# Kernel tuning notes

Measured on AMD Instinct MI355X. Metric: run time of the kernel, lower is better.

Reference implementation:

```python
import jax, jax.numpy as jnp
import numpy as np

N_NODES = 100000
N_EDGES = 600000
N_GRAPHS = 512
X_DIM = 2
E_DIM = 2
U_DIM = 2


def setup_inputs() -> dict:
    key = jax.random.key(0)
    ks = jax.random.split(key, 16)
    inp = {
        "x": jax.random.normal(ks[0], (N_NODES, X_DIM), jnp.float32),
        "edge_index": jax.random.randint(ks[1], (2, N_EDGES), 0, N_NODES, jnp.int64),
        "edge_attr": jax.random.normal(ks[2], (N_EDGES, E_DIM), jnp.float32),
        "u": jax.random.normal(ks[3], (N_GRAPHS, U_DIM), jnp.float32),
        "batch": jnp.sort(jax.random.randint(ks[4], (N_NODES,), 0, N_GRAPHS, jnp.int64)),
    }
    def lin(k, fin, fout):
        bound = 1.0 / np.sqrt(fin)
        kw, kb = jax.random.split(k)
        W = jax.random.uniform(kw, (fin, fout), jnp.float32, -bound, bound)
        b = jax.random.uniform(kb, (fout,), jnp.float32, -bound, bound)
        return W, b
    inp["W1a"], inp["b1a"] = lin(ks[5], X_DIM + E_DIM, 64)
    inp["W1b"], inp["b1b"] = lin(ks[6], 64, 128)
    inp["W2a"], inp["b2a"] = lin(ks[7], X_DIM + 128 + U_DIM, 256)
    inp["W2b"], inp["b2b"] = lin(ks[8], 256, 512)
    return inp


def reference(x, edge_index, edge_attr, u, batch, W1a, b1a, W1b, b1b, W2a, b2a, W2b, b2b):
    row, col = edge_index[0], edge_index[1]
    n = x.shape[0]
    # gather + concat -> MLP1 over edges: [E, 4] -> [E, 128]
    e_in = jnp.concatenate([x[col], edge_attr], axis=1)
    h = jnp.maximum(e_in @ W1a + b1a, 0.0) @ W1b + b1b
    # scatter_mean over destination nodes (row)
    s = jax.ops.segment_sum(h, row, num_segments=n)
    cnt = jax.ops.segment_sum(jnp.ones((row.shape[0], 1), h.dtype), row, num_segments=n)
    agg = s / jnp.maximum(cnt, 1.0)
    # node-level concat -> MLP2: [N, 132] -> [N, 512]
    z = jnp.concatenate([x, agg, u[batch]], axis=1)
    return jnp.maximum(z @ W2a + b2a, 0.0) @ W2b + b2b
```

## Files before the change

kernel.cpp:

```cpp
#include <hip/hip_runtime.h>

#define NN 100000
#define NE 600000
#define NP 100096
#define NB 391
#define NBE 9375

typedef float v4    __attribute__((ext_vector_type(4)));
typedef float f32x4 __attribute__((ext_vector_type(4)));
typedef short s16x4 __attribute__((ext_vector_type(4)));
typedef short s16x8 __attribute__((ext_vector_type(8)));

__device__ __forceinline__ short f2bf(float f) {
    unsigned u = __float_as_uint(f);
    u = (u + 0x7fffu + ((u >> 16) & 1u)) >> 16;
    return (short)u;
}
__device__ __forceinline__ float bf2f(unsigned short v) {
    return __uint_as_float(((unsigned)v) << 16);
}

__global__ __launch_bounds__(256) void hist_kernel(const int* __restrict__ ei,
                                                   int* __restrict__ deg) {
    int e = blockIdx.x * 256 + threadIdx.x;
    if (e < NE) atomicAdd(&deg[ei[e]], 1);
}

__global__ __launch_bounds__(256) void scan1_kernel(const int* __restrict__ deg,
                                                    int* __restrict__ partial,
                                                    int* __restrict__ bsum) {
    __shared__ int tmp[256];
    int t = threadIdx.x;
    int i = blockIdx.x * 256 + t;
    int v = deg[i];
    tmp[t] = v;
    __syncthreads();
    for (int off = 1; off < 256; off <<= 1) {
        int add = (t >= off) ? tmp[t - off] : 0;
        __syncthreads();
        tmp[t] += add;
        __syncthreads();
    }
    partial[i] = tmp[t] - v;
    if (t == 255) bsum[blockIdx.x] = tmp[255];
}

__global__ __launch_bounds__(512) void scan2_kernel(const int* __restrict__ bsum,
                                                    int* __restrict__ boff) {
    __shared__ int tmp[512];
    int t = threadIdx.x;
    int v = (t < NB) ? bsum[t] : 0;
    tmp[t] = v;
    __syncthreads();
    for (int off = 1; off < 512; off <<= 1) {
        int add = (t >= off) ? tmp[t - off] : 0;
        __syncthreads();
        tmp[t] += add;
        __syncthreads();
    }
    boff[t] = tmp[t] - v;
}

__global__ __launch_bounds__(256) void fill_kernel(const int* __restrict__ ei,
                                                   const float* __restrict__ x,
                                                   const float* __restrict__ ea,
                                                   const int* __restrict__ partial,
                                                   const int* __restrict__ boff,
                                                   int* __restrict__ cnt2,
                                                   int* __restrict__ rowp,
                                                   short* __restrict__ in_csr) {
    int e = blockIdx.x * 256 + threadIdx.x;
    if (e < NE) {
        int r = ei[e];
        int c = ei[NE + e];
        int p = partial[r] + boff[r >> 8] + atomicAdd(&cnt2[r], 1);
        rowp[p] = r;
        s16x8 v = {0, 0, 0, 0, 0, 0, 0, 0};
        v[0] = f2bf(x[2 * c]);  v[1] = f2bf(x[2 * c + 1]);
        v[2] = f2bf(ea[2 * e]); v[3] = f2bf(ea[2 * e + 1]);
        *(s16x8*)&in_csr[(size_t)p * 8] = v;
    }
}

__global__ __launch_bounds__(256) void zero_empty_kernel(const int* __restrict__ deg,
                                                         short* __restrict__ aggb) {
    int n = blockIdx.x * 256 + threadIdx.x;
    if (n < NN && deg[n] == 0) {
        s16x8 z = {0, 0, 0, 0, 0, 0, 0, 0};
        short* dst = aggb + (size_t)n * 128;
#pragma unroll
        for (int j = 0; j < 16; ++j) *(s16x8*)&dst[j * 8] = z;
    }
}

__global__ __launch_bounds__(256) void prep_kernel(const float* __restrict__ W2a,
                                                   const float* __restrict__ W2b,
                                                   const float* __restrict__ W1a,
                                                   const float* __restrict__ W1b,
                                                   short* __restrict__ W2aF,
                                                   short* __restrict__ W2bF,
                                                   short* __restrict__ W1aT,
                                                   short* __restrict__ W1bT) {
    int idx = blockIdx.x * 256 + threadIdx.x;
    if (idx < 16 * 5 * 512) {
        int j = idx & 7;
        int lane = (idx >> 3) & 63;
        int t2 = idx >> 9;
        int ks = t2 % 5, nb = t2 / 5;
        int n = nb * 16 + (lane & 15);
        int k = ks * 32 + (lane >> 4) * 8 + j;
        float v = 0.f;
        if (k < 128)       v = W2a[(2 + k) * 256 + n];
        else if (k == 128) v = W2a[0 * 256 + n];
        else if (k == 129) v = W2a[1 * 256 + n];
        else if (k == 130) v = W2a[130 * 256 + n];
        else if (k == 131) v = W2a[131 * 256 + n];
        W2aF[idx] = f2bf(v);
    }
    if (idx < 32 * 8 * 512) {
        int j = idx & 7;
        int lane = (idx >> 3) & 63;
        int t2 = idx >> 9;
        int ks = t2 & 7, nb = t2 >> 3;
        int n = nb * 16 + (lane & 15);
        int k = ks * 32 + (lane >> 4) * 8 + j;
        W2bF[idx] = f2bf(W2b[k * 512 + n]);
    }
    if (idx < 64 * 32) {
        int n = idx >> 5, k = idx & 31;
        W1aT[idx] = (k < 4) ? f2bf(W1a[k * 64 + n]) : (short)0;
    }
    if (idx < 128 * 64) {
        int n = idx >> 6, k = idx & 63;
        W1bT[idx] = f2bf(W1b[k * 128 + n]);
    }
}

__global__ __launch_bounds__(256) void edge_fused_kernel(
    const short* __restrict__ in_csr, const int* __restrict__ rowp,
    const short* __restrict__ W1aT, const short* __restrict__ W1bT,
    const float* __restrict__ b1a, const float* __restrict__ b1b,
    const int* __restrict__ partial, const int* __restrict__ boff,
    const int* __restrict__ deg,
    short* __restrict__ aggb, float* __restrict__ pstart,
    float* __restrict__ pend, int* __restrict__ eid)
{
    __shared__ short in[64 * 48];
    __shared__ short t1[64 * 72];
    __shared__ short hbf[64 * 136];
    __shared__ int   rows[64];
    __shared__ float midlo[128], midhi[128];
    const int tid = threadIdx.x;
    const int p0 = blockIdx.x * 64;

    if (tid < 64) {
        *(s16x8*)&in[tid * 48] = *(const s16x8*)&in_csr[(size_t)(p0 + tid) * 8];
        rows[tid] = rowp[p0 + tid];
    } else {
        int t2 = tid - 64;
        int r = t2 / 3, ch = t2 % 3;
        s16x8 z = {0, 0, 0, 0, 0, 0, 0, 0};
        *(s16x8*)&in[r * 48 + 8 + ch * 8] = z;
    }
    __syncthreads();

    const int lane = tid & 63, nw = tid >> 6;
    const int l15 = lane & 15, lk = lane >> 4;

    f32x4 a1[4];
#pragma unroll
    for (int bf = 0; bf < 4; ++bf) a1[bf] = (f32x4){0.f, 0.f, 0.f, 0.f};
    {
        s16x8 wA = *(const s16x8*)&W1aT[(nw * 16 + l15) * 32 + lk * 8];
#pragma unroll
        for (int bf = 0; bf < 4; ++bf) {
            s16x8 bI = *(const s16x8*)&in[(bf * 16 + l15) * 48 + lk * 8];
            a1[bf] = __builtin_amdgcn_mfma_f32_16x16x32_bf16(wA, bI, a1[bf], 0, 0, 0);
        }
    }
    {
        f32x4 bias = *(const f32x4*)&b1a[nw * 16 + lk * 4];
#pragma unroll
        for (int bf = 0; bf < 4; ++bf) {
            s16x4 pk;
#pragma unroll
            for (int j = 0; j < 4; ++j)
                pk[j] = f2bf(fmaxf(a1[bf][j] + bias[j], 0.f));
            *(s16x4*)&t1[(bf * 16 + l15) * 72 + nw * 16 + lk * 4] = pk;
        }
    }
    __syncthreads();

    f32x4 a2[2][4];
#pragma unroll
    for (int af = 0; af < 2; ++af)
#pragma unroll
        for (int bf = 0; bf < 4; ++bf) a2[af][bf] = (f32x4){0.f, 0.f, 0.f, 0.f};

#pragma unroll
    for (int ks = 0; ks < 2; ++ks) {
        s16x8 w[2], b[4];
#pragma unroll
        for (int af = 0; af < 2; ++af)
            w[af] = *(const s16x8*)&W1bT[((nw * 2 + af) * 16 + l15) * 64 + ks * 32 + lk * 8];
#pragma unroll
        for (int bf = 0; bf < 4; ++bf)
            b[bf] = *(const s16x8*)&t1[(bf * 16 + l15) * 72 + ks * 32 + lk * 8];
#pragma unroll
        for (int af = 0; af < 2; ++af)
#pragma unroll
            for (int bf = 0; bf < 4; ++bf)
                a2[af][bf] = __builtin_amdgcn_mfma_f32_16x16x32_bf16(
                    w[af], b[bf], a2[af][bf], 0, 0, 0);
    }
#pragma unroll
    for (int af = 0; af < 2; ++af) {
        int oc0 = (nw * 2 + af) * 16 + lk * 4;
        f32x4 bias = *(const f32x4*)&b1b[oc0];
#pragma unroll
        for (int bf = 0; bf < 4; ++bf) {
            s16x4 pk;
#pragma unroll
            for (int j = 0; j < 4; ++j)
                pk[j] = f2bf(a2[af][bf][j] + bias[j]);
            *(s16x4*)&hbf[(bf * 16 + l15) * 136 + oc0] = pk;
        }
    }
    __syncthreads();

    {
        const int half = tid >> 7;
        const int c = tid & 127;
        const int slo = half * 32, shi = slo + 32;
        float sum = 0.f;
        int cur = rows[slo];
        bool first = true;
        for (int i = slo; i < shi; ++i) {
            sum += bf2f((unsigned short)hbf[i * 136 + c]);
            bool segend = (i == shi - 1) || (rows[i + 1] != cur);
            if (segend) {
                bool crossMid  = (half == 0) && (i == 31) && (rows[32] == cur);
                bool fromLower = (half == 1) && first && (rows[31] == cur);
                if (crossMid) {
                    midlo[c] = sum;
                } else if (fromLower) {
                    midhi[c] = sum;
                } else {
                    int bs = partial[cur] + boff[cur >> 8];
                    int d = deg[cur];
                    bool sh = bs >= p0, eh = bs + d <= p0 + 64;
                    if (sh && eh)      aggb[(size_t)cur * 128 + c] = f2bf(sum / (float)d);
                    else if (sh)       pend[(size_t)blockIdx.x * 128 + c] = sum;
                    else if (eh)       pstart[(size_t)blockIdx.x * 128 + c] = sum;
                }
                sum = 0.f;
                first = false;
                if (i < shi - 1) cur = rows[i + 1];
            }
        }
    }
    __syncthreads();
    if (tid < 128 && rows[31] == rows[32]) {
        int c = tid, cur = rows[32];
        float s = midlo[c] + midhi[c];
        int bs = partial[cur] + boff[cur >> 8];
        int d = deg[cur];
        bool sh = bs >= p0, eh = bs + d <= p0 + 64;
        if (sh && eh)      aggb[(size_t)cur * 128 + c] = f2bf(s / (float)d);
        else if (sh)       pend[(size_t)blockIdx.x * 128 + c] = s;
        else if (eh)       pstart[(size_t)blockIdx.x * 128 + c] = s;
    }
    if (tid == 0) {
        int nlast = rows[63];
        int bs = partial[nlast] + boff[nlast >> 8];
        eid[blockIdx.x] = (bs + deg[nlast] > p0 + 64) ? nlast : -1;
    }
}

__global__ __launch_bounds__(128) void fixup_kernel(
    const float* __restrict__ pend, const float* __restrict__ pstart,
    const int* __restrict__ eid, const int* __restrict__ deg,
    short* __restrict__ aggb)
{
    int k = blockIdx.x;
    int n = eid[k];
    if (n < 0) return;
    int c = threadIdx.x;
    float s = pend[(size_t)k * 128 + c] + pstart[(size_t)(k + 1) * 128 + c];
    aggb[(size_t)n * 128 + c] = f2bf(s / (float)deg[n]);
}

__global__ __launch_bounds__(512, 4) void node_mfma_kernel(
    const float* __restrict__ x, const float* __restrict__ u,
    const int* __restrict__ batch,
    const short* __restrict__ aggb,
    const short* __restrict__ W2aF, const short* __restrict__ W2bF,
    const float* __restrict__ b2a, const float* __restrict__ b2b,
    float* __restrict__ out)
{
    __shared__ short lds[64 * 256];
    const int tid = threadIdx.x;
    const int node0 = blockIdx.x * 64;

#pragma unroll
    for (int it = 0; it < 2; ++it) {
        int idx = it * 512 + tid;
        int r = idx >> 4, ch = idx & 15;
        int node = node0 + r;
        s16x8 v = {0, 0, 0, 0, 0, 0, 0, 0};
        if (node < NN) v = *(const s16x8*)&aggb[(size_t)node * 128 + ch * 8];
        int sw = (ch & ~7) | ((ch ^ r) & 7);
        *(s16x8*)&lds[r * 192 + sw * 8] = v;
    }
    if (tid < 64) {
        int r = tid, node = node0 + r;
        s16x8 p = {0, 0, 0, 0, 0, 0, 0, 0};
        if (node < NN) {
            p[0] = f2bf(x[node * 2]); p[1] = f2bf(x[node * 2 + 1]);
            int b = batch[node];
            p[2] = f2bf(u[b * 2]); p[3] = f2bf(u[b * 2 + 1]);
        }
        int sw = 16 | (r & 7);
        *(s16x8*)&lds[r * 192 + sw * 8] = p;
    } else if (tid < 256) {
        int t2 = tid - 64;
        int r = t2 & 63;
        int ch = 17 + (t2 >> 6);
        int sw = (ch & ~7) | ((ch ^ r) & 7);
        s16x8 zz = {0, 0, 0, 0, 0, 0, 0, 0};
        *(s16x8*)&lds[r * 192 + sw * 8] = zz;
    }
    __syncthreads();

    const int lane = tid & 63, nw = tid >> 6;
    const int l15 = lane & 15, lk = lane >> 4;

    f32x4 acc1[4][2];
#pragma unroll
    for (int mf = 0; mf < 4; ++mf)
#pragma unroll
        for (int nf = 0; nf < 2; ++nf)
            acc1[mf][nf] = (f32x4){0.f, 0.f, 0.f, 0.f};

#pragma unroll
    for (int ks = 0; ks < 5; ++ks) {
        s16x8 a[4], w[2];
        int cb = ks * 4 + lk;
#pragma unroll
        for (int mf = 0; mf < 4; ++mf) {
            int r = mf * 16 + l15;
            int sw = (cb & ~7) | ((cb ^ r) & 7);
            a[mf] = *(const s16x8*)&lds[r * 192 + sw * 8];
        }
#pragma unroll
        for (int nf = 0; nf < 2; ++nf)
            w[nf] = *(const s16x8*)&W2aF[((((nw * 2 + nf) * 5) + ks) * 64 + lane) * 8];
#pragma unroll
        for (int mf = 0; mf < 4; ++mf)
#pragma unroll
            for (int nf = 0; nf < 2; ++nf)
                acc1[mf][nf] = __builtin_amdgcn_mfma_f32_16x16x32_bf16(
                    w[nf], a[mf], acc1[mf][nf], 0, 0, 0);
    }
    __syncthreads();

#pragma unroll
    for (int nf = 0; nf < 2; ++nf) {
        int n0 = nw * 32 + nf * 16 + lk * 4;
        f32x4 bias = *(const f32x4*)&b2a[n0];
        int ch = n0 >> 3, off = n0 & 7;
#pragma unroll
        for (int mf = 0; mf < 4; ++mf) {
            int m = mf * 16 + l15;
            s16x4 pk;
#pragma unroll
            for (int j = 0; j < 4; ++j)
                pk[j] = f2bf(fmaxf(acc1[mf][nf][j] + bias[j], 0.f));
            int sw = (ch & ~7) | ((ch ^ m) & 7);
            *(s16x4*)&lds[m * 256 + sw * 8 + off] = pk;
        }
    }
    __syncthreads();

    f32x4 acc2[4][4];
#pragma unroll
    for (int mf = 0; mf < 4; ++mf)
#pragma unroll
        for (int nf = 0; nf < 4; ++nf)
            acc2[mf][nf] = (f32x4){0.f, 0.f, 0.f, 0.f};

#pragma unroll
    for (int ks = 0; ks < 8; ++ks) {
        s16x8 b[4], w[4];
        int cb = ks * 4 + lk;
#pragma unroll
        for (int mf = 0; mf < 4; ++mf) {
            int r = mf * 16 + l15;
            int sw = (cb & ~7) | ((cb ^ r) & 7);
            b[mf] = *(const s16x8*)&lds[r * 256 + sw * 8];
        }
#pragma unroll
        for (int nf = 0; nf < 4; ++nf)
            w[nf] = *(const s16x8*)&W2bF[((((nw * 4 + nf) * 8) + ks) * 64 + lane) * 8];
#pragma unroll
        for (int mf = 0; mf < 4; ++mf)
#pragma unroll
            for (int nf = 0; nf < 4; ++nf)
                acc2[mf][nf] = __builtin_amdgcn_mfma_f32_16x16x32_bf16(
                    w[nf], b[mf], acc2[mf][nf], 0, 0, 0);
    }

#pragma unroll
    for (int nf = 0; nf < 4; ++nf) {
        int n0 = nw * 64 + nf * 16 + lk * 4;
        f32x4 bias = *(const f32x4*)&b2b[n0];
#pragma unroll
        for (int mf = 0; mf < 4; ++mf) {
            int node = node0 + mf * 16 + l15;
            if (node < NN) {
                f32x4 o = acc2[mf][nf] + bias;
                *(f32x4*)&out[(size_t)node * 512 + n0] = o;
            }
        }
    }
}

extern "C" void kernel_launch(void* const* d_in, const int* in_sizes, int n_in,
                              void* d_out, int out_size, void* d_ws, size_t ws_size,
                              hipStream_t stream) {
    const float* x          = (const float*)d_in[0];
    const int*   edge_index = (const int*)d_in[1];
    const float* edge_attr  = (const float*)d_in[2];
    const float* u          = (const float*)d_in[3];
    const int*   batch      = (const int*)d_in[4];
    const float* W1a        = (const float*)d_in[5];
    const float* b1a        = (const float*)d_in[6];
    const float* W1b        = (const float*)d_in[7];
    const float* b1b        = (const float*)d_in[8];
    const float* W2a        = (const float*)d_in[9];
    const float* b2a        = (const float*)d_in[10];
    const float* W2b        = (const float*)d_in[11];
    const float* b2b        = (const float*)d_in[12];
    float* out = (float*)d_out;

    short* aggb   = (short*)d_ws;
    short* W2aF   = aggb + (size_t)NN * 128;
    short* W2bF   = W2aF + 16 * 5 * 512;
    short* W1aT   = W2bF + 32 * 8 * 512;
    short* W1bT   = W1aT + 64 * 32;
    int*   deg    = (int*)(W1bT + 128 * 64);
    int*   cnt2   = deg + NP;
    int*   partial= cnt2 + NP;
    int*   bsum   = partial + NP;
    int*   boff   = bsum + 512;
    int*   rowp   = boff + 512;
    int*   eid    = rowp + NE;
    float* pstart = (float*)(eid + NBE);
    float* pend   = pstart + (size_t)NBE * 128;
    short* in_csr = (short*)(pend + (size_t)NBE * 128);

    hipMemsetAsync(deg, 0, 2 * NP * sizeof(int), stream);

    prep_kernel <<<512, 256, 0, stream>>>(W2a, W2b, W1a, W1b,
                                          W2aF, W2bF, W1aT, W1bT);
    hist_kernel <<<(NE + 255) / 256, 256, 0, stream>>>(edge_index, deg);
    scan1_kernel<<<NB, 256, 0, stream>>>(deg, partial, bsum);
    scan2_kernel<<<1, 512, 0, stream>>>(bsum, boff);
    fill_kernel <<<(NE + 255) / 256, 256, 0, stream>>>(edge_index, x, edge_attr,
                                                       partial, boff, cnt2,
                                                       rowp, in_csr);
    zero_empty_kernel<<<NB, 256, 0, stream>>>(deg, aggb);

    edge_fused_kernel<<<NBE, 256, 0, stream>>>(
        in_csr, rowp, W1aT, W1bT, b1a, b1b,
        partial, boff, deg, aggb, pstart, pend, eid);

    fixup_kernel<<<NBE - 1, 128, 0, stream>>>(pend, pstart, eid, deg, aggb);

    node_mfma_kernel<<<(NN + 63) / 64, 512, 0, stream>>>(
        x, u, batch, aggb, W2aF, W2bF, b2a, b2b, out);
}
```

Measured before the change: 244.3 us.

## Fold prep, empty-zeroing and boundary fixup into neighbouring kernels

Merges weight preparation into the histogram kernel, removes the empty-node zeroing kernel and the boundary fixup kernel. The node kernel now reads each node's degree and CSR offset, loads aggregated rows directly, and zeros empty nodes or combines the split partial sums across block boundaries itself. This removes three launches and a pass over aggregation memory, at the cost of extra index loads and a sync in the node kernel.

```diff
diff --git a/kernel.cpp b/kernel.cpp
--- a/kernel.cpp
+++ b/kernel.cpp
@@ -20,10 +20,48 @@
     return __uint_as_float(((unsigned)v) << 16);
 }
 
-__global__ __launch_bounds__(256) void hist_kernel(const int* __restrict__ ei,
-                                                   int* __restrict__ deg) {
-    int e = blockIdx.x * 256 + threadIdx.x;
-    if (e < NE) atomicAdd(&deg[ei[e]], 1);
+__global__ __launch_bounds__(256) void hist_prep_kernel(
+    const int* __restrict__ ei, int* __restrict__ deg,
+    const float* __restrict__ W2a, const float* __restrict__ W2b,
+    const float* __restrict__ W1a, const float* __restrict__ W1b,
+    short* __restrict__ W2aF, short* __restrict__ W2bF,
+    short* __restrict__ W1aT, short* __restrict__ W1bT)
+{
+    int idx = blockIdx.x * 256 + threadIdx.x;
+    if (idx < NE) atomicAdd(&deg[ei[idx]], 1);
+
+    if (idx < 16 * 5 * 512) {
+        int j = idx & 7;
+        int lane = (idx >> 3) & 63;
+        int t2 = idx >> 9;
+        int ks = t2 % 5, nb = t2 / 5;
+        int n = nb * 16 + (lane & 15);
+        int k = ks * 32 + (lane >> 4) * 8 + j;
+        float v = 0.f;
+        if (k < 128)       v = W2a[(2 + k) * 256 + n];
+        else if (k == 128) v = W2a[0 * 256 + n];
+        else if (k == 129) v = W2a[1 * 256 + n];
+        else if (k == 130) v = W2a[130 * 256 + n];
+        else if (k == 131) v = W2a[131 * 256 + n];
+        W2aF[idx] = f2bf(v);
+    }
+    if (idx < 32 * 8 * 512) {
+        int j = idx & 7;
+        int lane = (idx >> 3) & 63;
+        int t2 = idx >> 9;
+        int ks = t2 & 7, nb = t2 >> 3;
+        int n = nb * 16 + (lane & 15);
+        int k = ks * 32 + (lane >> 4) * 8 + j;
+        W2bF[idx] = f2bf(W2b[k * 512 + n]);
+    }
+    if (idx < 64 * 32) {
+        int n = idx >> 5, k = idx & 31;
+        W1aT[idx] = (k < 4) ? f2bf(W1a[k * 64 + n]) : (short)0;
+    }
+    if (idx < 128 * 64) {
+        int n = idx >> 6, k = idx & 63;
+        W1bT[idx] = f2bf(W1b[k * 128 + n]);
+    }
 }
 
 __global__ __launch_bounds__(256) void scan1_kernel(const int* __restrict__ deg,
@@ -82,60 +120,6 @@
     }
 }
 
-__global__ __launch_bounds__(256) void zero_empty_kernel(const int* __restrict__ deg,
-                                                         short* __restrict__ aggb) {
-    int n = blockIdx.x * 256 + threadIdx.x;
-    if (n < NN && deg[n] == 0) {
-        s16x8 z = {0, 0, 0, 0, 0, 0, 0, 0};
-        short* dst = aggb + (size_t)n * 128;
-#pragma unroll
-        for (int j = 0; j < 16; ++j) *(s16x8*)&dst[j * 8] = z;
-    }
-}
-
-__global__ __launch_bounds__(256) void prep_kernel(const float* __restrict__ W2a,
-                                                   const float* __restrict__ W2b,
-                                                   const float* __restrict__ W1a,
-                                                   const float* __restrict__ W1b,
-                                                   short* __restrict__ W2aF,
-                                                   short* __restrict__ W2bF,
-                                                   short* __restrict__ W1aT,
-                                                   short* __restrict__ W1bT) {
-    int idx = blockIdx.x * 256 + threadIdx.x;
-    if (idx < 16 * 5 * 512) {
-        int j = idx & 7;
-        int lane = (idx >> 3) & 63;
-        int t2 = idx >> 9;
-        int ks = t2 % 5, nb = t2 / 5;
-        int n = nb * 16 + (lane & 15);
-        int k = ks * 32 + (lane >> 4) * 8 + j;
-        float v = 0.f;
-        if (k < 128)       v = W2a[(2 + k) * 256 + n];
-        else if (k == 128) v = W2a[0 * 256 + n];
-        else if (k == 129) v = W2a[1 * 256 + n];
-        else if (k == 130) v = W2a[130 * 256 + n];
-        else if (k == 131) v = W2a[131 * 256 + n];
-        W2aF[idx] = f2bf(v);
-    }
-    if (idx < 32 * 8 * 512) {
-        int j = idx & 7;
-        int lane = (idx >> 3) & 63;
-        int t2 = idx >> 9;
-        int ks = t2 & 7, nb = t2 >> 3;
-        int n = nb * 16 + (lane & 15);
-        int k = ks * 32 + (lane >> 4) * 8 + j;
-        W2bF[idx] = f2bf(W2b[k * 512 + n]);
-    }
-    if (idx < 64 * 32) {
-        int n = idx >> 5, k = idx & 31;
-        W1aT[idx] = (k < 4) ? f2bf(W1a[k * 64 + n]) : (short)0;
-    }
-    if (idx < 128 * 64) {
-        int n = idx >> 6, k = idx & 63;
-        W1bT[idx] = f2bf(W1b[k * 128 + n]);
-    }
-}
-
 __global__ __launch_bounds__(256) void edge_fused_kernel(
     const short* __restrict__ in_csr, const int* __restrict__ rowp,
     const short* __restrict__ W1aT, const short* __restrict__ W1bT,
@@ -143,7 +127,7 @@
     const int* __restrict__ partial, const int* __restrict__ boff,
     const int* __restrict__ deg,
     short* __restrict__ aggb, float* __restrict__ pstart,
-    float* __restrict__ pend, int* __restrict__ eid)
+    float* __restrict__ pend)
 {
     __shared__ short in[64 * 48];
     __shared__ short t1[64 * 72];
@@ -270,45 +254,61 @@
         else if (sh)       pend[(size_t)blockIdx.x * 128 + c] = s;
         else if (eh)       pstart[(size_t)blockIdx.x * 128 + c] = s;
     }
-    if (tid == 0) {
-        int nlast = rows[63];
-        int bs = partial[nlast] + boff[nlast >> 8];
-        eid[blockIdx.x] = (bs + deg[nlast] > p0 + 64) ? nlast : -1;
-    }
-}
-
-__global__ __launch_bounds__(128) void fixup_kernel(
-    const float* __restrict__ pend, const float* __restrict__ pstart,
-    const int* __restrict__ eid, const int* __restrict__ deg,
-    short* __restrict__ aggb)
-{
-    int k = blockIdx.x;
-    int n = eid[k];
-    if (n < 0) return;
-    int c = threadIdx.x;
-    float s = pend[(size_t)k * 128 + c] + pstart[(size_t)(k + 1) * 128 + c];
-    aggb[(size_t)n * 128 + c] = f2bf(s / (float)deg[n]);
 }
 
 __global__ __launch_bounds__(512, 4) void node_mfma_kernel(
     const float* __restrict__ x, const float* __restrict__ u,
     const int* __restrict__ batch,
     const short* __restrict__ aggb,
+    const int* __restrict__ deg, const int* __restrict__ partial,
+    const int* __restrict__ boff,
+    const float* __restrict__ pstart, const float* __restrict__ pend,
     const short* __restrict__ W2aF, const short* __restrict__ W2bF,
     const float* __restrict__ b2a, const float* __restrict__ b2b,
     float* __restrict__ out)
 {
     __shared__ short lds[64 * 256];
+    __shared__ int   rmode[64];
+    __shared__ float rinv[64];
+    __shared__ int   rk[64];
     const int tid = threadIdx.x;
     const int node0 = blockIdx.x * 64;
+
+    if (tid < 64) {
+        int node = node0 + tid;
+        int mode = 0, k = 0;
+        float inv = 0.f;
+        if (node < NN) {
+            int d = deg[node];
+            if (d > 0) {
+                int bs = partial[node] + boff[node >> 8];
+                k = bs >> 6;
+                mode = ((bs & 63) + d > 64) ? 2 : 1;
+                inv = 1.0f / (float)d;
+            }
+        }
+        rmode[tid] = mode; rinv[tid] = inv; rk[tid] = k;
+    }
+    __syncthreads();
 
 #pragma unroll
     for (int it = 0; it < 2; ++it) {
         int idx = it * 512 + tid;
         int r = idx >> 4, ch = idx & 15;
         int node = node0 + r;
+        int mode = rmode[r];
         s16x8 v = {0, 0, 0, 0, 0, 0, 0, 0};
-        if (node < NN) v = *(const s16x8*)&aggb[(size_t)node * 128 + ch * 8];
+        if (mode == 1) {
+            v = *(const s16x8*)&aggb[(size_t)node * 128 + ch * 8];
+        } else if (mode == 2) {
+            float inv = rinv[r];
+            int k = rk[r];
+            const float* pe = &pend[(size_t)k * 128 + ch * 8];
+            const float* ps = &pstart[(size_t)(k + 1) * 128 + ch * 8];
+#pragma unroll
+            for (int j = 0; j < 8; ++j)
+                v[j] = f2bf((pe[j] + ps[j]) * inv);
+        }
         int sw = (ch & ~7) | ((ch ^ r) & 7);
         *(s16x8*)&lds[r * 192 + sw * 8] = v;
     }
@@ -454,29 +454,25 @@
     int*   bsum   = partial + NP;
     int*   boff   = bsum + 512;
     int*   rowp   = boff + 512;
-    int*   eid    = rowp + NE;
-    float* pstart = (float*)(eid + NBE);
+    float* pstart = (float*)(rowp + NE);
     float* pend   = pstart + (size_t)NBE * 128;
     short* in_csr = (short*)(pend + (size_t)NBE * 128);
 
     hipMemsetAsync(deg, 0, 2 * NP * sizeof(int), stream);
 
-    prep_kernel <<<512, 256, 0, stream>>>(W2a, W2b, W1a, W1b,
-                                          W2aF, W2bF, W1aT, W1bT);
-    hist_kernel <<<(NE + 255) / 256, 256, 0, stream>>>(edge_index, deg);
+    hist_prep_kernel<<<(NE + 255) / 256, 256, 0, stream>>>(
+        edge_index, deg, W2a, W2b, W1a, W1b, W2aF, W2bF, W1aT, W1bT);
     scan1_kernel<<<NB, 256, 0, stream>>>(deg, partial, bsum);
     scan2_kernel<<<1, 512, 0, stream>>>(bsum, boff);
     fill_kernel <<<(NE + 255) / 256, 256, 0, stream>>>(edge_index, x, edge_attr,
                                                        partial, boff, cnt2,
                                                        rowp, in_csr);
-    zero_empty_kernel<<<NB, 256, 0, stream>>>(deg, aggb);
 
     edge_fused_kernel<<<NBE, 256, 0, stream>>>(
         in_csr, rowp, W1aT, W1bT, b1a, b1b,
-        partial, boff, deg, aggb, pstart, pend, eid);
-
-    fixup_kernel<<<NBE - 1, 128, 0, stream>>>(pend, pstart, eid, deg, aggb);
+        partial, boff, deg, aggb, pstart, pend);
 
     node_mfma_kernel<<<(NN + 63) / 64, 512, 0, stream>>>(
-        x, u, batch, aggb, W2aF, W2bF, b2a, b2b, out);
-}
+        x, u, batch, aggb, deg, partial, boff, pstart, pend,
+        W2aF, W2bF, b2a, b2b, out);
+}
```

Result: faster. 231.1 us (-5.4%).
